# Kernel tuning notes

Measured on AMD Instinct MI355X. Metric: run time of the kernel, lower is better.

The kernel has to match this reference:

```python
import jax, jax.numpy as jnp
import numpy as np

N = 20000      # nodes
E = 640000     # edges (before self-loops)
F = 64         # base node feature len
H = 2          # heads per layer
EPS = 1e-5
NEG_SLOPE = 0.2  # PyG GATConv leaky_relu slope


def setup_inputs():
    key = jax.random.key(0)
    ks = jax.random.split(key, 16)
    s = 0.1
    x = jax.random.normal(ks[0], (N, F), jnp.float32)
    edge_index = jax.random.randint(ks[1], (2, E), 0, N, dtype=jnp.int64)
    # layer 1: in=F, heads=H, out-per-head C1=F -> out dim H*F=128
    C1 = F
    W1 = jax.random.normal(ks[2], (F, H * C1), jnp.float32) * s
    att_src1 = jax.random.normal(ks[3], (H, C1), jnp.float32) * s
    att_dst1 = jax.random.normal(ks[4], (H, C1), jnp.float32) * s
    bias1 = jnp.zeros((H * C1,), jnp.float32)
    gamma1 = jnp.ones((H * C1,), jnp.float32)
    beta1 = jnp.zeros((H * C1,), jnp.float32)
    # layer 2: in=H*F=128, heads=H, out-per-head C2=H*F -> out dim H*H*F=256
    C2 = H * F
    W2 = jax.random.normal(ks[5], (H * C1, H * C2), jnp.float32) * s
    att_src2 = jax.random.normal(ks[6], (H, C2), jnp.float32) * s
    att_dst2 = jax.random.normal(ks[7], (H, C2), jnp.float32) * s
    bias2 = jnp.zeros((H * C2,), jnp.float32)
    gamma2 = jnp.ones((H * C2,), jnp.float32)
    beta2 = jnp.zeros((H * C2,), jnp.float32)
    return {"x": x, "edge_index": edge_index,
            "W1": W1, "att_src1": att_src1, "att_dst1": att_dst1, "bias1": bias1,
            "gamma1": gamma1, "beta1": beta1,
            "W2": W2, "att_src2": att_src2, "att_dst2": att_dst2, "bias2": bias2,
            "gamma2": gamma2, "beta2": beta2}


def _gat_conv(x, src, dst, W, att_src, att_dst, bias):
    # PyG GATConv (concat=True, add_self_loops already applied to src/dst)
    n = x.shape[0]
    h, c = att_src.shape
    hx = (x @ W).reshape(n, h, c)                       # [N,H,C]
    a_s = jnp.einsum('nhc,hc->nh', hx, att_src)         # [N,H]
    a_d = jnp.einsum('nhc,hc->nh', hx, att_dst)
    e = a_s[src] + a_d[dst]                             # [E',H]
    e = jnp.where(e > 0, e, NEG_SLOPE * e)              # leaky relu
    # segment softmax over incoming edges of each target node
    m = jax.ops.segment_max(e, dst, num_segments=n)     # [N,H]
    p = jnp.exp(e - m[dst])
    z = jax.ops.segment_sum(p, dst, num_segments=n)     # [N,H]
    alpha = p / z[dst]                                  # [E',H]
    msg = hx[src] * alpha[:, :, None]                   # [E',H,C]
    out = jax.ops.segment_sum(msg, dst, num_segments=n) # [N,H,C]
    return out.reshape(n, h * c) + bias


def _batch_norm(x, gamma, beta):
    mu = x.mean(axis=0)
    var = x.var(axis=0)  # biased, matches torch BN normalization
    return (x - mu) * jax.lax.rsqrt(var + EPS) * gamma + beta


def reference(x, edge_index, W1, att_src1, att_dst1, bias1, gamma1, beta1,
              W2, att_src2, att_dst2, bias2, gamma2, beta2):
    loops = jnp.arange(N, dtype=edge_index.dtype)
    src = jnp.concatenate([edge_index[0], loops])
    dst = jnp.concatenate([edge_index[1], loops])
    h = _gat_conv(x, src, dst, W1, att_src1, att_dst1, bias1)
    h = jax.nn.relu(_batch_norm(h, gamma1, beta1))
    h = _gat_conv(h, src, dst, W2, att_src2, att_dst2, bias2)
    h = jax.nn.relu(_batch_norm(h, gamma2, beta2))
    return h
```

## Files before the change

### kernel.cpp

```cpp
#include <hip/hip_runtime.h>
#include <hip/hip_bf16.h>
#include <math.h>

#define NN 20000
#define ER 640000
#define ET 660000
#define D1 128
#define D2 256
#define EPSV 1e-5f
#define SLOPE 0.2f
#define NT1 313
#define MAXD 256
#define NCH 256
#define CHE 2500

typedef __attribute__((ext_vector_type(8))) short bf16x8;
typedef __attribute__((ext_vector_type(4))) float f32x4;

__device__ __forceinline__ int detect64(const void* ei) {
  const int* p = (const int*)ei;
  return (p[1] | p[3] | p[5] | p[7]) == 0;
}
__device__ __forceinline__ int clampn(int v) { return v < 0 ? 0 : (v >= NN ? NN-1 : v); }
__device__ __forceinline__ float bf16_lo(unsigned int u){ return __uint_as_float(u<<16); }
__device__ __forceinline__ float bf16_hi(unsigned int u){ return __uint_as_float(u & 0xffff0000u); }

__global__ __launch_bounds__(256) void k_init(const void* ei, unsigned int* dpart, float* bnz,
                                              const float* W1, const float* W2,
                                              __hip_bfloat16* w1bT, __hip_bfloat16* w2bT) {
  __shared__ unsigned int lds[10256];
  int b = blockIdx.x, t = threadIdx.x;
  if (b < NCH) {
    for (int i = t; i < 10000; i += 256) lds[i] = 0;
    __syncthreads();
    int base = b * CHE;
    if (detect64(ei)) {
      const long long* q = (const long long*)ei + ER;
      for (int i = base + t; i < base + CHE; i += 256) {
        int d = clampn((int)q[i]);
        atomicAdd(&lds[d>>1], 1u << ((d&1)*16));
      }
    } else {
      const int* q = (const int*)ei + ER;
      for (int i = base + t; i < base + CHE; i += 256) {
        int d = clampn(q[i]);
        atomicAdd(&lds[d>>1], 1u << ((d&1)*16));
      }
    }
    __syncthreads();
    for (int i = t; i < 10000; i += 256) dpart[(size_t)b*10000 + i] = lds[i];
    return;
  }
  if (b < NCH + 3) {
    int gid = (b - NCH)*256 + t;
    if (gid < 768) bnz[gid] = 0.f;
    return;
  }
  float* tf = (float*)lds;
  int pb = b - NCH - 3;
  if (pb == 0) {
    for (int i = t; i < 8192; i += 256)
      tf[(i >> 7)*129 + (i & 127)] = W1[i];
    __syncthreads();
    for (int i = t; i < 8192; i += 256) {
      int n = i >> 6, k = i & 63;
      w1bT[i] = __float2bfloat16(tf[k*129 + n]);
    }
  } else {
    int k0 = (pb - 1) * 32;
    for (int i = t; i < 8192; i += 256) {
      int kk = i >> 8, n = i & 255;
      tf[kk*257 + n] = W2[(k0 + kk)*256 + n];
    }
    __syncthreads();
    for (int i = t; i < 8192; i += 256) {
      int n = i >> 5, kk = i & 31;
      w2bT[n*128 + k0 + kk] = __float2bfloat16(tf[kk*257 + n]);
    }
  }
}

__global__ __launch_bounds__(256) void k_prefix(unsigned short* dp, int* endv, int* srcs) {
  int n = blockIdx.x*256 + threadIdx.x;
  if (n >= NN) return;
  int run = 1;
  for (int c = 0; c < NCH; c++) {
    int idx = c*20000 + n;
    int v = dp[idx];
    dp[idx] = (unsigned short)run;
    run += v;
  }
  if (run > MAXD) run = MAXD;
  endv[n] = n*MAXD + run;
  srcs[n*MAXD] = n;
}

__global__ __launch_bounds__(256) void k_gs(const float* x, const __hip_bfloat16* w1bT,
                                            const float* att_s1, const float* att_d1,
                                            __hip_bfloat16* hxb, float2* as1, float2* ad1,
                                            const void* ei, const unsigned int* bases, int* srcs) {
  __shared__ unsigned int cnt[10000];
  __shared__ __hip_bfloat16 As[64][72];
  __shared__ float asred[4][64], adred[4][64];
  int b = blockIdx.x, t = threadIdx.x;
  if (b >= NT1) {
    int sb = b - NT1;
    for (int i = t; i < 10000; i += 256) cnt[i] = bases[(size_t)sb*10000 + i];
    __syncthreads();
    int base = sb * CHE;
    if (detect64(ei)) {
      const long long* ps = (const long long*)ei;
      const long long* pd = ps + ER;
      #pragma unroll 4
      for (int i = base + t; i < base + CHE; i += 256) {
        int s = clampn((int)ps[i]);
        int d = clampn((int)pd[i]);
        unsigned int old = atomicAdd(&cnt[d>>1], 1u << ((d&1)*16));
        unsigned int f = (old >> ((d&1)*16)) & 0xffffu;
        if (f < MAXD) srcs[d*MAXD + (int)f] = s;
      }
    } else {
      const int* ps = (const int*)ei;
      const int* pd = ps + ER;
      #pragma unroll 4
      for (int i = base + t; i < base + CHE; i += 256) {
        int s = clampn(ps[i]);
        int d = clampn(pd[i]);
        unsigned int old = atomicAdd(&cnt[d>>1], 1u << ((d&1)*16));
        unsigned int f = (old >> ((d&1)*16)) & 0xffffu;
        if (f < MAXD) srcs[d*MAXD + (int)f] = s;
      }
    }
    return;
  }
  int m0 = b * 64;
  for (int i = t; i < 512; i += 256) {
    int r = i >> 3, s = i & 7;
    int gr = m0 + r; if (gr >= NN) gr = NN - 1;
    float4 f0 = ((const float4*)(x + (size_t)gr*64))[s*2];
    float4 f1 = ((const float4*)(x + (size_t)gr*64))[s*2+1];
    __hip_bfloat16 hb[8] = {
      __float2bfloat16(f0.x), __float2bfloat16(f0.y), __float2bfloat16(f0.z), __float2bfloat16(f0.w),
      __float2bfloat16(f1.x), __float2bfloat16(f1.y), __float2bfloat16(f1.z), __float2bfloat16(f1.w)};
    *(uint4*)&As[r][s*8] = *(uint4*)hb;
  }
  __syncthreads();
  int w = t >> 6, lane = t & 63, lm = lane & 15, q = lane >> 4;
  f32x4 acc[4][2];
  #pragma unroll
  for (int rt = 0; rt < 4; rt++)
    #pragma unroll
    for (int ct = 0; ct < 2; ct++) acc[rt][ct] = (f32x4){0.f,0.f,0.f,0.f};
  #pragma unroll
  for (int kc = 0; kc < 2; kc++) {
    bf16x8 bfr[2];
    #pragma unroll
    for (int ct = 0; ct < 2; ct++)
      bfr[ct] = *(const bf16x8*)(w1bT + (size_t)(w*32 + ct*16 + lm)*64 + kc*32 + q*8);
    #pragma unroll
    for (int rt = 0; rt < 4; rt++) {
      bf16x8 a = *(const bf16x8*)&As[rt*16 + lm][kc*32 + q*8];
      acc[rt][0] = __builtin_amdgcn_mfma_f32_16x16x32_bf16(a, bfr[0], acc[rt][0], 0, 0, 0);
      acc[rt][1] = __builtin_amdgcn_mfma_f32_16x16x32_bf16(a, bfr[1], acc[rt][1], 0, 0, 0);
    }
  }
  #pragma unroll
  for (int rt = 0; rt < 4; rt++)
    #pragma unroll
    for (int ct = 0; ct < 2; ct++)
      #pragma unroll
      for (int rg = 0; rg < 4; rg++) {
        int row = m0 + rt*16 + q*4 + rg;
        int col = w*32 + ct*16 + lm;
        if (row < NN) hxb[(size_t)row*128 + col] = __float2bfloat16(acc[rt][ct][rg]);
      }
  float asc[2], adc[2];
  #pragma unroll
  for (int ct = 0; ct < 2; ct++) {
    int col = w*32 + ct*16 + lm;
    asc[ct] = att_s1[col]; adc[ct] = att_d1[col];
  }
  #pragma unroll
  for (int rt = 0; rt < 4; rt++)
    #pragma unroll
    for (int rg = 0; rg < 4; rg++) {
      float ps = acc[rt][0][rg]*asc[0] + acc[rt][1][rg]*asc[1];
      float pd = acc[rt][0][rg]*adc[0] + acc[rt][1][rg]*adc[1];
      #pragma unroll
      for (int o = 1; o < 16; o <<= 1) { ps += __shfl_xor(ps, o); pd += __shfl_xor(pd, o); }
      if (lm == 0) { int row = rt*16 + q*4 + rg; asred[w][row] = ps; adred[w][row] = pd; }
    }
  __syncthreads();
  if (t < 64) {
    int row = m0 + t;
    if (row < NN) {
      as1[row] = make_float2(asred[0][t] + asred[1][t], asred[2][t] + asred[3][t]);
      ad1[row] = make_float2(adred[0][t] + adred[1][t], adred[2][t] + adred[3][t]);
    }
  }
}

__global__ __launch_bounds__(256) void k_gemm2f(const float* out1, const __hip_bfloat16* w2bT,
                                                const float* bns1, const float* bnq1,
                                                const float* gamma1, const float* beta1,
                                                const float* att_s2, const float* att_d2,
                                                __hip_bfloat16* hxb, float2* as2, float2* ad2) {
  __shared__ __hip_bfloat16 As[64][136];
  __shared__ float AB[2][128];
  __shared__ float asred[4][64], adred[4][64];
  int t = threadIdx.x;
  int m0 = blockIdx.x * 64;
  if (t < 128) {
    float mean = bns1[t]*(1.f/NN);
    float var  = bnq1[t]*(1.f/NN) - mean*mean;
    float A = rsqrtf(var + EPSV)*gamma1[t];
    AB[0][t] = A; AB[1][t] = beta1[t] - mean*A;
  }
  __syncthreads();
  for (int i = t; i < 1024; i += 256) {
    int r = i >> 4, s = i & 15;
    int gr = m0 + r; if (gr >= NN) gr = NN - 1;
    float4 f0 = ((const float4*)(out1 + (size_t)gr*128))[s*2];
    float4 f1 = ((const float4*)(out1 + (size_t)gr*128))[s*2+1];
    int c = s*8;
    float v[8] = {f0.x,f0.y,f0.z,f0.w,f1.x,f1.y,f1.z,f1.w};
    __hip_bfloat16 hb[8];
    #pragma unroll
    for (int k = 0; k < 8; k++)
      hb[k] = __float2bfloat16(fmaxf(v[k]*AB[0][c+k] + AB[1][c+k], 0.f));
    *(uint4*)&As[r][s*8] = *(uint4*)hb;
  }
  __syncthreads();
  int w = t >> 6, lane = t & 63, lm = lane & 15, q = lane >> 4;
  f32x4 acc[4][4];
  #pragma unroll
  for (int rt = 0; rt < 4; rt++)
    #pragma unroll
    for (int ct = 0; ct < 4; ct++) acc[rt][ct] = (f32x4){0.f,0.f,0.f,0.f};
  #pragma unroll
  for (int kc = 0; kc < 4; kc++) {
    bf16x8 bfr[4];
    #pragma unroll
    for (int ct = 0; ct < 4; ct++)
      bfr[ct] = *(const bf16x8*)(w2bT + (size_t)(w*64 + ct*16 + lm)*128 + kc*32 + q*8);
    #pragma unroll
    for (int rt = 0; rt < 4; rt++) {
      bf16x8 a = *(const bf16x8*)&As[rt*16 + lm][kc*32 + q*8];
      #pragma unroll
      for (int ct = 0; ct < 4; ct++)
        acc[rt][ct] = __builtin_amdgcn_mfma_f32_16x16x32_bf16(a, bfr[ct], acc[rt][ct], 0, 0, 0);
    }
  }
  #pragma unroll
  for (int rt = 0; rt < 4; rt++)
    #pragma unroll
    for (int ct = 0; ct < 4; ct++)
      #pragma unroll
      for (int rg = 0; rg < 4; rg++) {
        int row = m0 + rt*16 + q*4 + rg;
        int col = w*64 + ct*16 + lm;
        if (row < NN) hxb[(size_t)row*256 + col] = __float2bfloat16(acc[rt][ct][rg]);
      }
  float asc[4], adc[4];
  #pragma unroll
  for (int ct = 0; ct < 4; ct++) {
    int col = w*64 + ct*16 + lm;
    asc[ct] = att_s2[col]; adc[ct] = att_d2[col];
  }
  #pragma unroll
  for (int rt = 0; rt < 4; rt++)
    #pragma unroll
    for (int rg = 0; rg < 4; rg++) {
      float ps = acc[rt][0][rg]*asc[0] + acc[rt][1][rg]*asc[1]
               + acc[rt][2][rg]*asc[2] + acc[rt][3][rg]*asc[3];
      float pd = acc[rt][0][rg]*adc[0] + acc[rt][1][rg]*adc[1]
               + acc[rt][2][rg]*adc[2] + acc[rt][3][rg]*adc[3];
      #pragma unroll
      for (int o = 1; o < 16; o <<= 1) { ps += __shfl_xor(ps, o); pd += __shfl_xor(pd, o); }
      if (lm == 0) { int row = rt*16 + q*4 + rg; asred[w][row] = ps; adred[w][row] = pd; }
    }
  __syncthreads();
  if (t < 64) {
    int row = m0 + t;
    if (row < NN) {
      as2[row] = make_float2(asred[0][t] + asred[1][t], asred[2][t] + asred[3][t]);
      ad2[row] = make_float2(adred[0][t] + adred[1][t], adred[2][t] + adred[3][t]);
    }
  }
}

__global__ __launch_bounds__(256) void k_agg1(const int* endv, const int* srcs,
                                              const float2* asv, const float2* adv,
                                              const uint4* hx, const float* bias, float* out) {
  int t = threadIdx.x;
  int n = blockIdx.x*4 + (t >> 6);
  int lane = t & 63;
  int el = lane >> 3, c = lane & 7;
  int h = c >> 2;
  float2 ad = adv[n];
  int beg = n * MAXD, end = endv[n];
  float a[16];
  #pragma unroll
  for (int k = 0; k < 16; k++) a[k] = 0.f;
  float z0 = 0.f, z1 = 0.f;
  for (int cb = beg; cb < end; cb += 64) {
    int len = end - cb; if (len > 64) len = 64;
    int s = 0; float p0 = 0.f, p1 = 0.f;
    if (lane < len) {
      s = srcs[cb + lane];
      float2 as = asv[s];
      float e0 = as.x + ad.x, e1 = as.y + ad.y;
      e0 = e0 > 0.f ? e0 : SLOPE*e0;
      e1 = e1 > 0.f ? e1 : SLOPE*e1;
      p0 = __expf(e0); p1 = __expf(e1);
      z0 += p0; z1 += p1;
    }
    #pragma unroll 2
    for (int j = 0; j < len; j += 8) {
      int e = j + el;
      int ec = e < len ? e : len-1;
      int se = __shfl(s, ec);
      float q0 = __shfl(p0, ec);
      float q1 = __shfl(p1, ec);
      float pj = e < len ? (h ? q1 : q0) : 0.f;
      const uint4* rp = hx + (size_t)se*16 + 2*c;
      uint4 u0 = rp[0];
      uint4 u1 = rp[1];
      a[0]  += pj*bf16_lo(u0.x); a[1]  += pj*bf16_hi(u0.x);
      a[2]  += pj*bf16_lo(u0.y); a[3]  += pj*bf16_hi(u0.y);
      a[4]  += pj*bf16_lo(u0.z); a[5]  += pj*bf16_hi(u0.z);
      a[6]  += pj*bf16_lo(u0.w); a[7]  += pj*bf16_hi(u0.w);
      a[8]  += pj*bf16_lo(u1.x); a[9]  += pj*bf16_hi(u1.x);
      a[10] += pj*bf16_lo(u1.y); a[11] += pj*bf16_hi(u1.y);
      a[12] += pj*bf16_lo(u1.z); a[13] += pj*bf16_hi(u1.z);
      a[14] += pj*bf16_lo(u1.w); a[15] += pj*bf16_hi(u1.w);
    }
  }
  #pragma unroll
  for (int k = 0; k < 16; k++) {
    a[k] += __shfl_down(a[k], 32);
    a[k] += __shfl_down(a[k], 16);
    a[k] += __shfl_down(a[k], 8);
  }
  #pragma unroll
  for (int o = 1; o < 64; o <<= 1) { z0 += __shfl_xor(z0, o); z1 += __shfl_xor(z1, o); }
  if (lane < 8) {
    float inv = 1.f / (h ? z1 : z0);
    float4* op = (float4*)(out + (size_t)n*D1 + 16*c);
    const float4* bp = (const float4*)(bias + 16*c);
    #pragma unroll
    for (int i = 0; i < 4; i++) {
      float4 bv = bp[i];
      float4 ov = { a[4*i]*inv + bv.x, a[4*i+1]*inv + bv.y,
                    a[4*i+2]*inv + bv.z, a[4*i+3]*inv + bv.w };
      op[i] = ov;
    }
  }
}

__global__ __launch_bounds__(256) void k_agg2(const int* endv, const int* srcs,
                                              const float2* asv, const float2* adv,
                                              const uint4* hx, const float* bias, float* out) {
  int t = threadIdx.x;
  int n = blockIdx.x*4 + (t >> 6);
  int lane = t & 63;
  int el = lane >> 4, c = lane & 15;
  int h = c >> 3;
  float2 ad = adv[n];
  int beg = n * MAXD, end = endv[n];
  float a[16];
  #pragma unroll
  for (int k = 0; k < 16; k++) a[k] = 0.f;
  float z0 = 0.f, z1 = 0.f;
  for (int cb = beg; cb < end; cb += 64) {
    int len = end - cb; if (len > 64) len = 64;
    int s = 0; float p0 = 0.f, p1 = 0.f;
    if (lane < len) {
      s = srcs[cb + lane];
      float2 as = asv[s];
      float e0 = as.x + ad.x, e1 = as.y + ad.y;
      e0 = e0 > 0.f ? e0 : SLOPE*e0;
      e1 = e1 > 0.f ? e1 : SLOPE*e1;
      p0 = __expf(e0); p1 = __expf(e1);
      z0 += p0; z1 += p1;
    }
    #pragma unroll 2
    for (int j = 0; j < len; j += 4) {
      int e = j + el;
      int ec = e < len ? e : len-1;
      int se = __shfl(s, ec);
      float q0 = __shfl(p0, ec);
      float q1 = __shfl(p1, ec);
      float pj = e < len ? (h ? q1 : q0) : 0.f;
      const uint4* rp = hx + (size_t)se*32 + 2*c;
      uint4 u0 = rp[0];
      uint4 u1 = rp[1];
      a[0]  += pj*bf16_lo(u0.x); a[1]  += pj*bf16_hi(u0.x);
      a[2]  += pj*bf16_lo(u0.y); a[3]  += pj*bf16_hi(u0.y);
      a[4]  += pj*bf16_lo(u0.z); a[5]  += pj*bf16_hi(u0.z);
      a[6]  += pj*bf16_lo(u0.w); a[7]  += pj*bf16_hi(u0.w);
      a[8]  += pj*bf16_lo(u1.x); a[9]  += pj*bf16_hi(u1.x);
      a[10] += pj*bf16_lo(u1.y); a[11] += pj*bf16_hi(u1.y);
      a[12] += pj*bf16_lo(u1.z); a[13] += pj*bf16_hi(u1.z);
      a[14] += pj*bf16_lo(u1.w); a[15] += pj*bf16_hi(u1.w);
    }
  }
  #pragma unroll
  for (int k = 0; k < 16; k++) {
    a[k] += __shfl_down(a[k], 32);
    a[k] += __shfl_down(a[k], 16);
  }
  #pragma unroll
  for (int o = 1; o < 64; o <<= 1) { z0 += __shfl_xor(z0, o); z1 += __shfl_xor(z1, o); }
  if (lane < 16) {
    float inv = 1.f / (h ? z1 : z0);
    float4* op = (float4*)(out + (size_t)n*D2 + 16*c);
    const float4* bp = (const float4*)(bias + 16*c);
    #pragma unroll
    for (int i = 0; i < 4; i++) {
      float4 bv = bp[i];
      float4 ov = { a[4*i]*inv + bv.x, a[4*i+1]*inv + bv.y,
                    a[4*i+2]*inv + bv.z, a[4*i+3]*inv + bv.w };
      op[i] = ov;
    }
  }
}

template<int D>
__global__ void k_bnstats(const float* x, float* bnsum, float* bnsq) {
  const int ROWS = 100;
  int c = threadIdx.x;
  int r0 = blockIdx.x * ROWS;
  float s = 0.f, s2 = 0.f;
  for (int r = 0; r < ROWS; r++) {
    float v = x[(size_t)(r0 + r)*D + c];
    s += v; s2 += v*v;
  }
  atomicAdd(&bnsum[c], s);
  atomicAdd(&bnsq[c], s2);
}

__global__ void k_bnapply2(const float* x, const float* bnsum, const float* bnsq,
                           const float* gamma, const float* beta, float* out) {
  int i = blockIdx.x*blockDim.x + threadIdx.x;
  if (i >= NN*D2/4) return;
  int c = (i & 63) * 4;
  float4 v = ((const float4*)x)[i];
  float r[4] = {v.x, v.y, v.z, v.w};
  #pragma unroll
  for (int k = 0; k < 4; k++) {
    float mean = bnsum[c+k] * (1.f/NN);
    float var  = bnsq[c+k] * (1.f/NN) - mean*mean;
    float o = (r[k] - mean) * rsqrtf(var + EPSV) * gamma[c+k] + beta[c+k];
    r[k] = o > 0.f ? o : 0.f;
  }
  float4 o4 = {r[0], r[1], r[2], r[3]};
  ((float4*)out)[i] = o4;
}

extern "C" void kernel_launch(void* const* d_in, const int* in_sizes, int n_in,
                              void* d_out, int out_size, void* d_ws, size_t ws_size,
                              hipStream_t stream) {
  const float* x      = (const float*)d_in[0];
  const void*  ei     = d_in[1];
  const float* W1     = (const float*)d_in[2];
  const float* att_s1 = (const float*)d_in[3];
  const float* att_d1 = (const float*)d_in[4];
  const float* bias1  = (const float*)d_in[5];
  const float* gamma1 = (const float*)d_in[6];
  const float* beta1  = (const float*)d_in[7];
  const float* W2     = (const float*)d_in[8];
  const float* att_s2 = (const float*)d_in[9];
  const float* att_d2 = (const float*)d_in[10];
  const float* bias2  = (const float*)d_in[11];
  const float* gamma2 = (const float*)d_in[12];
  const float* beta2  = (const float*)d_in[13];

  char* p = (char*)d_ws;
  __hip_bfloat16* hx1b = (__hip_bfloat16*)p; p += (size_t)NN*D1*2;
  __hip_bfloat16* hx2b = (__hip_bfloat16*)p; p += (size_t)NN*D2*2;
  float* out1 = (float*)p; p += (size_t)NN*D1*4;
  float* out2 = (float*)p; p += (size_t)NN*D2*4;
  float2* as1 = (float2*)p; p += (size_t)NN*8;
  float2* ad1 = (float2*)p; p += (size_t)NN*8;
  float2* as2 = (float2*)p; p += (size_t)NN*8;
  float2* ad2 = (float2*)p; p += (size_t)NN*8;
  float* bns1 = (float*)p; p += D1*4;
  float* bnq1 = (float*)p; p += D1*4;
  float* bns2 = (float*)p; p += D2*4;
  float* bnq2 = (float*)p; p += D2*4;
  int* endv   = (int*)p; p += (size_t)NN*4;
  unsigned int* dpart = (unsigned int*)p; p += (size_t)NCH*10000*4;
  int* srcs   = (int*)p; p += (size_t)NN*MAXD*4;
  __hip_bfloat16* w1bT = (__hip_bfloat16*)p; p += 128*64*2;
  __hip_bfloat16* w2bT = (__hip_bfloat16*)p; p += 256*128*2;

  k_init<<<NCH + 8, 256, 0, stream>>>(ei, dpart, bns1, W1, W2, w1bT, w2bT);
  k_prefix<<<(NN+255)/256, 256, 0, stream>>>((unsigned short*)dpart, endv, srcs);
  k_gs<<<NT1 + NCH, 256, 0, stream>>>(x, w1bT, att_s1, att_d1, hx1b, as1, ad1,
                                      ei, dpart, srcs);
  k_agg1<<<NN/4, 256, 0, stream>>>(endv, srcs, as1, ad1, (const uint4*)hx1b, bias1, out1);
  k_bnstats<D1><<<200, D1, 0, stream>>>(out1, bns1, bnq1);
  k_gemm2f<<<(NN+63)/64, 256, 0, stream>>>(out1, w2bT, bns1, bnq1, gamma1, beta1,
                                           att_s2, att_d2, hx2b, as2, ad2);
  k_agg2<<<NN/4, 256, 0, stream>>>(endv, srcs, as2, ad2, (const uint4*)hx2b, bias2, out2);
  k_bnstats<D2><<<200, D2, 0, stream>>>(out2, bns2, bnq2);
  k_bnapply2<<<(NN*D2/4 + 255)/256, 256, 0, stream>>>(out2, bns2, bnq2, gamma2, beta2,
                                                      (float*)d_out);
}
```

Measured before the change: 231.3 us.

## Replace two-pass CSR build with single-pass grouped edge buckets

Drops the separate degree-count pass in k_init and the serial k_prefix kernel. Edges are now scattered in one pass by 8 large groups, each writing into a fixed 32-slot bucket per destination node and recording per-group counts. The aggregation kernels rebuild a small 8-entry prefix per node and map each edge index to its bucket slot. This removes a kernel launch and a long serial per-node loop over 256 chunks. In exchange, only 8 blocks do the scatter, so it has far less parallelism, and every edge lookup in the aggregation kernels now pays extra index arithmetic.

```diff
diff --git a/kernel.cpp b/kernel.cpp
--- a/kernel.cpp
+++ b/kernel.cpp
@@ -4,15 +4,15 @@
 
 #define NN 20000
 #define ER 640000
-#define ET 660000
 #define D1 128
 #define D2 256
 #define EPSV 1e-5f
 #define SLOPE 0.2f
 #define NT1 313
-#define MAXD 256
-#define NCH 256
-#define CHE 2500
+#define NGR 8
+#define GSL 32
+#define NSTR 272
+#define GEC (ER/NGR)
 
 typedef __attribute__((ext_vector_type(8))) short bf16x8;
 typedef __attribute__((ext_vector_type(4))) float f32x4;
@@ -25,39 +25,16 @@
 __device__ __forceinline__ float bf16_lo(unsigned int u){ return __uint_as_float(u<<16); }
 __device__ __forceinline__ float bf16_hi(unsigned int u){ return __uint_as_float(u & 0xffff0000u); }
 
-__global__ __launch_bounds__(256) void k_init(const void* ei, unsigned int* dpart, float* bnz,
-                                              const float* W1, const float* W2,
+__global__ __launch_bounds__(256) void k_init(float* bnz, const float* W1, const float* W2,
                                               __hip_bfloat16* w1bT, __hip_bfloat16* w2bT) {
-  __shared__ unsigned int lds[10256];
+  __shared__ float tf[8256];
   int b = blockIdx.x, t = threadIdx.x;
-  if (b < NCH) {
-    for (int i = t; i < 10000; i += 256) lds[i] = 0;
-    __syncthreads();
-    int base = b * CHE;
-    if (detect64(ei)) {
-      const long long* q = (const long long*)ei + ER;
-      for (int i = base + t; i < base + CHE; i += 256) {
-        int d = clampn((int)q[i]);
-        atomicAdd(&lds[d>>1], 1u << ((d&1)*16));
-      }
-    } else {
-      const int* q = (const int*)ei + ER;
-      for (int i = base + t; i < base + CHE; i += 256) {
-        int d = clampn(q[i]);
-        atomicAdd(&lds[d>>1], 1u << ((d&1)*16));
-      }
-    }
-    __syncthreads();
-    for (int i = t; i < 10000; i += 256) dpart[(size_t)b*10000 + i] = lds[i];
-    return;
-  }
-  if (b < NCH + 3) {
-    int gid = (b - NCH)*256 + t;
+  if (b < 3) {
+    int gid = b*256 + t;
     if (gid < 768) bnz[gid] = 0.f;
     return;
   }
-  float* tf = (float*)lds;
-  int pb = b - NCH - 3;
+  int pb = b - 3;
   if (pb == 0) {
     for (int i = t; i < 8192; i += 256)
       tf[(i >> 7)*129 + (i & 127)] = W1[i];
@@ -80,60 +57,45 @@
   }
 }
 
-__global__ __launch_bounds__(256) void k_prefix(unsigned short* dp, int* endv, int* srcs) {
-  int n = blockIdx.x*256 + threadIdx.x;
-  if (n >= NN) return;
-  int run = 1;
-  for (int c = 0; c < NCH; c++) {
-    int idx = c*20000 + n;
-    int v = dp[idx];
-    dp[idx] = (unsigned short)run;
-    run += v;
-  }
-  if (run > MAXD) run = MAXD;
-  endv[n] = n*MAXD + run;
-  srcs[n*MAXD] = n;
-}
-
 __global__ __launch_bounds__(256) void k_gs(const float* x, const __hip_bfloat16* w1bT,
                                             const float* att_s1, const float* att_d1,
                                             __hip_bfloat16* hxb, float2* as1, float2* ad1,
-                                            const void* ei, const unsigned int* bases, int* srcs) {
+                                            const void* ei, unsigned int* gcnt, int* srcs) {
   __shared__ unsigned int cnt[10000];
   __shared__ __hip_bfloat16 As[64][72];
   __shared__ float asred[4][64], adred[4][64];
   int b = blockIdx.x, t = threadIdx.x;
-  if (b >= NT1) {
-    int sb = b - NT1;
-    for (int i = t; i < 10000; i += 256) cnt[i] = bases[(size_t)sb*10000 + i];
+  if (b < NGR) {
+    int g = b;
+    for (int i = t; i < 10000; i += 256) cnt[i] = 0;
     __syncthreads();
-    int base = sb * CHE;
+    int base = g * GEC;
     if (detect64(ei)) {
       const long long* ps = (const long long*)ei;
       const long long* pd = ps + ER;
-      #pragma unroll 4
-      for (int i = base + t; i < base + CHE; i += 256) {
+      for (int i = base + t; i < base + GEC; i += 256) {
         int s = clampn((int)ps[i]);
         int d = clampn((int)pd[i]);
         unsigned int old = atomicAdd(&cnt[d>>1], 1u << ((d&1)*16));
         unsigned int f = (old >> ((d&1)*16)) & 0xffffu;
-        if (f < MAXD) srcs[d*MAXD + (int)f] = s;
+        if (f < GSL) srcs[(size_t)d*NSTR + 1 + g*GSL + (int)f] = s;
       }
     } else {
       const int* ps = (const int*)ei;
       const int* pd = ps + ER;
-      #pragma unroll 4
-      for (int i = base + t; i < base + CHE; i += 256) {
+      for (int i = base + t; i < base + GEC; i += 256) {
         int s = clampn(ps[i]);
         int d = clampn(pd[i]);
         unsigned int old = atomicAdd(&cnt[d>>1], 1u << ((d&1)*16));
         unsigned int f = (old >> ((d&1)*16)) & 0xffffu;
-        if (f < MAXD) srcs[d*MAXD + (int)f] = s;
+        if (f < GSL) srcs[(size_t)d*NSTR + 1 + g*GSL + (int)f] = s;
       }
     }
+    __syncthreads();
+    for (int i = t; i < 10000; i += 256) gcnt[(size_t)g*10000 + i] = cnt[i];
     return;
   }
-  int m0 = b * 64;
+  int m0 = (b - NGR) * 64;
   for (int i = t; i < 512; i += 256) {
     int r = i >> 3, s = i & 7;
     int gr = m0 + r; if (gr >= NN) gr = NN - 1;
@@ -289,7 +251,27 @@
   }
 }
 
-__global__ __launch_bounds__(256) void k_agg1(const int* endv, const int* srcs,
+#define GROUP_PREFIX(gcnt, n, P, total)                          \
+  int P[9]; P[0] = 0;                                            \
+  {                                                              \
+    int sh_ = ((n) & 1) * 16, ix_ = (n) >> 1;                    \
+    _Pragma("unroll")                                            \
+    for (int g_ = 0; g_ < NGR; g_++) {                           \
+      int cg_ = (gcnt[g_*10000 + ix_] >> sh_) & 0xffff;          \
+      if (cg_ > GSL) cg_ = GSL;                                  \
+      P[g_+1] = P[g_] + cg_;                                     \
+    }                                                            \
+  }                                                              \
+  int total = 1 + P[NGR];
+
+__device__ __forceinline__ int edge_addr(const int* P, int n, int u) {
+  int g = 0, Pg = 0;
+  #pragma unroll
+  for (int gg = 1; gg < NGR; gg++) { int c2 = u >= P[gg]; g += c2; Pg = c2 ? P[gg] : Pg; }
+  return n*NSTR + 1 + g*GSL + (u - Pg);
+}
+
+__global__ __launch_bounds__(256) void k_agg1(const unsigned int* gcnt, const int* srcs,
                                               const float2* asv, const float2* adv,
                                               const uint4* hx, const float* bias, float* out) {
   int t = threadIdx.x;
@@ -298,16 +280,17 @@
   int el = lane >> 3, c = lane & 7;
   int h = c >> 2;
   float2 ad = adv[n];
-  int beg = n * MAXD, end = endv[n];
+  GROUP_PREFIX(gcnt, n, P, total);
   float a[16];
   #pragma unroll
   for (int k = 0; k < 16; k++) a[k] = 0.f;
   float z0 = 0.f, z1 = 0.f;
-  for (int cb = beg; cb < end; cb += 64) {
-    int len = end - cb; if (len > 64) len = 64;
+  for (int cb = 0; cb < total; cb += 64) {
+    int len = total - cb; if (len > 64) len = 64;
     int s = 0; float p0 = 0.f, p1 = 0.f;
     if (lane < len) {
-      s = srcs[cb + lane];
+      int e = cb + lane;
+      s = (e == 0) ? n : srcs[edge_addr(P, n, e - 1)];
       float2 as = asv[s];
       float e0 = as.x + ad.x, e1 = as.y + ad.y;
       e0 = e0 > 0.f ? e0 : SLOPE*e0;
@@ -358,7 +341,7 @@
   }
 }
 
-__global__ __launch_bounds__(256) void k_agg2(const int* endv, const int* srcs,
+__global__ __launch_bounds__(256) void k_agg2(const unsigned int* gcnt, const int* srcs,
                                               const float2* asv, const float2* adv,
                                               const uint4* hx, const float* bias, float* out) {
   int t = threadIdx.x;
@@ -367,16 +350,17 @@
   int el = lane >> 4, c = lane & 15;
   int h = c >> 3;
   float2 ad = adv[n];
-  int beg = n * MAXD, end = endv[n];
+  GROUP_PREFIX(gcnt, n, P, total);
   float a[16];
   #pragma unroll
   for (int k = 0; k < 16; k++) a[k] = 0.f;
   float z0 = 0.f, z1 = 0.f;
-  for (int cb = beg; cb < end; cb += 64) {
-    int len = end - cb; if (len > 64) len = 64;
+  for (int cb = 0; cb < total; cb += 64) {
+    int len = total - cb; if (len > 64) len = 64;
     int s = 0; float p0 = 0.f, p1 = 0.f;
     if (lane < len) {
-      s = srcs[cb + lane];
+      int e = cb + lane;
+      s = (e == 0) ? n : srcs[edge_addr(P, n, e - 1)];
       float2 as = asv[s];
       float e0 = as.x + ad.x, e1 = as.y + ad.y;
       e0 = e0 > 0.f ? e0 : SLOPE*e0;
@@ -489,21 +473,19 @@
   float* bnq1 = (float*)p; p += D1*4;
   float* bns2 = (float*)p; p += D2*4;
   float* bnq2 = (float*)p; p += D2*4;
-  int* endv   = (int*)p; p += (size_t)NN*4;
-  unsigned int* dpart = (unsigned int*)p; p += (size_t)NCH*10000*4;
-  int* srcs   = (int*)p; p += (size_t)NN*MAXD*4;
+  unsigned int* gcnt = (unsigned int*)p; p += (size_t)NGR*10000*4;
+  int* srcs   = (int*)p; p += (size_t)NN*NSTR*4;
   __hip_bfloat16* w1bT = (__hip_bfloat16*)p; p += 128*64*2;
   __hip_bfloat16* w2bT = (__hip_bfloat16*)p; p += 256*128*2;
 
-  k_init<<<NCH + 8, 256, 0, stream>>>(ei, dpart, bns1, W1, W2, w1bT, w2bT);
-  k_prefix<<<(NN+255)/256, 256, 0, stream>>>((unsigned short*)dpart, endv, srcs);
-  k_gs<<<NT1 + NCH, 256, 0, stream>>>(x, w1bT, att_s1, att_d1, hx1b, as1, ad1,
-                                      ei, dpart, srcs);
-  k_agg1<<<NN/4, 256, 0, stream>>>(endv, srcs, as1, ad1, (const uint4*)hx1b, bias1, out1);
+  k_init<<<8, 256, 0, stream>>>(bns1, W1, W2, w1bT, w2bT);
+  k_gs<<<NGR + NT1, 256, 0, stream>>>(x, w1bT, att_s1, att_d1, hx1b, as1, ad1,
+                                      ei, gcnt, srcs);
+  k_agg1<<<NN/4, 256, 0, stream>>>(gcnt, srcs, as1, ad1, (const uint4*)hx1b, bias1, out1);
   k_bnstats<D1><<<200, D1, 0, stream>>>(out1, bns1, bnq1);
   k_gemm2f<<<(NN+63)/64, 256, 0, stream>>>(out1, w2bT, bns1, bnq1, gamma1, beta1,
                                            att_s2, att_d2, hx2b, as2, ad2);
-  k_agg2<<<NN/4, 256, 0, stream>>>(endv, srcs, as2, ad2, (const uint4*)hx2b, bias2, out2);
+  k_agg2<<<NN/4, 256, 0, stream>>>(gcnt, srcs, as2, ad2, (const uint4*)hx2b, bias2, out2);
   k_bnstats<D2><<<200, D2, 0, stream>>>(out2, bns2, bnq2);
   k_bnapply2<<<(NN*D2/4 + 255)/256, 256, 0, stream>>>(out2, bns2, bnq2, gamma2, beta2,
                                                       (float*)d_out);
```

Result: slower. 403.3 us (+74.4%).
